# Performance work log

Measured on AMD Instinct MI355X. Metric: run time of the kernel, lower is better.

Reference implementation:

```python
import jax, jax.numpy as jnp
import numpy as np

EMBED = 2048
HEADS = 16
GROUPS = 4
HEAD_DIM = EMBED // HEADS  # 128
REPEATS = HEADS // GROUPS  # 4


def setup_inputs() -> dict:
    key = jax.random.key(0)
    ks = jax.random.split(key, 9)
    s = 1.0 / np.sqrt(EMBED)
    kv_dim = GROUPS * HEAD_DIM
    return {
        "x": jax.random.normal(ks[0], (2, 2048, EMBED), dtype=jnp.float32),
        "Wq": jax.random.normal(ks[1], (EMBED, EMBED), dtype=jnp.float32) * s,
        "bq": jnp.zeros((EMBED,), dtype=jnp.float32),
        "Wk": jax.random.normal(ks[2], (EMBED, kv_dim), dtype=jnp.float32) * s,
        "bk": jnp.zeros((kv_dim,), dtype=jnp.float32),
        "Wv": jax.random.normal(ks[3], (EMBED, kv_dim), dtype=jnp.float32) * s,
        "bv": jnp.zeros((kv_dim,), dtype=jnp.float32),
        "Wo": jax.random.normal(ks[4], (EMBED, EMBED), dtype=jnp.float32) * s,
        "bo": jnp.zeros((EMBED,), dtype=jnp.float32),
    }


def reference(x, Wq, bq, Wk, bk, Wv, bv, Wo, bo):
    b, t, e = x.shape
    q = x @ Wq + bq                                   # [b,t,e]
    k = x @ Wk + bk                                   # [b,t,g*d]
    v = x @ Wv + bv
    # [b, g, r, t, d] for q; [b, g, t, d] for k,v (repeat_interleave == group-major)
    q = q.reshape(b, t, GROUPS, REPEATS, HEAD_DIM).transpose(0, 2, 3, 1, 4)
    k = k.reshape(b, t, GROUPS, HEAD_DIM).transpose(0, 2, 1, 3)
    v = v.reshape(b, t, GROUPS, HEAD_DIM).transpose(0, 2, 1, 3)
    scale = 1.0 / np.sqrt(HEAD_DIM)
    scores = jnp.einsum('bgrqd,bgkd->bgrqk', q, k) * scale
    causal = jnp.tril(jnp.ones((t, t), dtype=bool))
    scores = jnp.where(causal, scores, -jnp.inf)
    w = jax.nn.softmax(scores, axis=-1)
    out = jnp.einsum('bgrqk,bgkd->bgrqd', w, v)       # [b,g,r,t,d]
    out = out.transpose(0, 3, 1, 2, 4).reshape(b, t, e)
    return out @ Wo + bo
```

## Files before the change

### kernel.cpp

```cpp
#include <hip/hip_runtime.h>
#include <cstdint>

typedef __bf16 bf16;
typedef __attribute__((ext_vector_type(8))) __bf16 bf16x8;
typedef __attribute__((ext_vector_type(4))) __bf16 bf16x4;
typedef __attribute__((ext_vector_type(4))) float f32x4;

__device__ __forceinline__ void load_lds16(const void* g, void* l) {
  __builtin_amdgcn_global_load_lds(
      (const __attribute__((address_space(1))) unsigned int*)g,
      (__attribute__((address_space(3))) unsigned int*)l, 16, 0, 0);
}

__device__ __forceinline__ float fast_exp2(float x) {
  float r;
  asm volatile("v_exp_f32 %0, %1" : "=v"(r) : "v"(x));
  return r;
}

template <bool OUT_F32>
__global__ __launch_bounds__(256) void gemm_bt(
    const bf16* __restrict__ A, const bf16* __restrict__ Bt,
    const float* __restrict__ bias, void* __restrict__ Cv,
    int M, int N, int K) {
  __shared__ __align__(16) bf16 sA[128 * 64];
  __shared__ __align__(16) bf16 sB[128 * 64];
  const int t = threadIdx.x;
  const int w = t >> 6, lane = t & 63;
  const int quad = lane >> 4, l16 = lane & 15;
  const int wm = (w >> 1) * 64, wn = (w & 1) * 64;
  const int bm = blockIdx.y * 128, bn = blockIdx.x * 128;

  f32x4 acc[4][4] = {};
  const int srow = lane >> 3;
  const int sg = lane & 7;

  for (int kt = 0; kt < (K >> 6); ++kt) {
    const int k0 = kt << 6;
#pragma unroll
    for (int c2 = 0; c2 < 4; ++c2) {
      int c = c2 * 4 + w;
      int row = c * 8 + srow;
      int gg = sg ^ (row & 7);
      load_lds16(A + (int64_t)(bm + row) * K + k0 + gg * 8, sA + c * 512);
      load_lds16(Bt + (int64_t)(bn + row) * K + k0 + gg * 8, sB + c * 512);
    }
    asm volatile("s_waitcnt vmcnt(0)" ::: "memory");
    __syncthreads();
#pragma unroll
    for (int ks = 0; ks < 2; ++ks) {
      bf16x8 af[4], bfr[4];
#pragma unroll
      for (int i = 0; i < 4; ++i) {
        int m = wm + i * 16 + l16;
        af[i] = *(const bf16x8*)(sA + m * 64 + (((ks * 4 + quad) ^ (l16 & 7)) * 8));
        int n = wn + i * 16 + l16;
        bfr[i] = *(const bf16x8*)(sB + n * 64 + (((ks * 4 + quad) ^ (l16 & 7)) * 8));
      }
#pragma unroll
      for (int i = 0; i < 4; ++i)
#pragma unroll
        for (int j = 0; j < 4; ++j)
          acc[i][j] = __builtin_amdgcn_mfma_f32_16x16x32_bf16(af[i], bfr[j],
                                                              acc[i][j], 0, 0, 0);
    }
    __syncthreads();
  }
#pragma unroll
  for (int i = 0; i < 4; ++i) {
    int gm = bm + wm + i * 16 + quad * 4;
#pragma unroll
    for (int j = 0; j < 4; ++j) {
      int gn = bn + wn + j * 16 + l16;
      float bvv = bias ? bias[gn] : 0.0f;
#pragma unroll
      for (int r = 0; r < 4; ++r) {
        float v = acc[i][j][r] + bvv;
        if (OUT_F32)
          ((float*)Cv)[(int64_t)(gm + r) * N + gn] = v;
        else
          ((bf16*)Cv)[(int64_t)(gm + r) * N + gn] = (bf16)v;
      }
    }
  }
}

__global__ __launch_bounds__(256, 2) void attn(
    const bf16* __restrict__ QKV, const bf16* __restrict__ Vt,
    bf16* __restrict__ Out) {
  constexpr float CC = 0.08838834764831845f * 1.44269504088896f;
  __shared__ __align__(16) bf16 sK[2][64 * 128];
  __shared__ __align__(16) bf16 sV[2][128 * 64];
  __shared__ __align__(16) bf16 sP[128 * 64];

  const int t = threadIdx.x;
  const int w = t >> 6, lane = t & 63;
  const int quad = lane >> 4, l16 = lane & 15;
  const int p = blockIdx.x, h = blockIdx.y, b = blockIdx.z;
  const int g = h >> 2;
  const int wr0 = w * 16;
  const int kbase = 2048 + g * 128;
  const bf16* vtb = Vt + (int64_t)((b * 4 + g) * 128) * 2048;
  const int rk = lane >> 4, rv = lane >> 3, sgv = lane & 7;
  const int qrow0A = p * 64, qrow0B = (31 - p) * 64;
  const int niters = 32 - p;

  bf16x8 qreg[2][4];
#pragma unroll
  for (int u = 0; u < 2; ++u) {
    int qr = (u == 0 ? qrow0A : qrow0B);
#pragma unroll
    for (int ks = 0; ks < 4; ++ks)
      qreg[u][ks] = *(const bf16x8*)(QKV +
          (int64_t)(b * 2048 + qr + wr0 + l16) * 3072 + h * 128 + ks * 32 +
          quad * 8);
  }

  f32x4 oacc[2][8] = {};
  float mrow[2] = {-3.0e38f, -3.0e38f};
  float lrow[2] = {0.f, 0.f};

  auto stage = [&](int n0, bf16* sKb, bf16* sVb) {
#pragma unroll
    for (int c2 = 0; c2 < 4; ++c2) {
      int c = c2 * 4 + w;
      int rowk = c * 4 + rk;
      int ggk = (l16 & 8) | ((l16 ^ rowk) & 7);
      load_lds16(QKV + (int64_t)(b * 2048 + n0 + rowk) * 3072 + kbase + ggk * 8,
                 sKb + c * 512);
      int rowv = c * 8 + rv;
      int ggv = sgv ^ (rowv & 7);
      load_lds16(vtb + (int64_t)rowv * 2048 + n0 + ggv * 8, sVb + c * 512);
    }
  };

  stage(0, sK[0], sV[0]);

  const int prowA = wr0 + l16;
  const int prowB = 64 + wr0 + l16;

  for (int it = 0; it < niters; ++it) {
    const int cur = it & 1;
    const int n0 = it * 64;
    bf16* sKc = sK[cur];
    bf16* sVc = sV[cur];
    const bool actA = (it <= p);

    asm volatile("s_waitcnt vmcnt(0)\n\ts_barrier" ::: "memory");
    if (it + 1 < niters) stage(n0 + 64, sK[cur ^ 1], sV[cur ^ 1]);

    f32x4 sacc[2][4] = {};
    if (actA) {
#pragma unroll
      for (int ks = 0; ks < 4; ++ks) {
        bf16x8 ak[4];
#pragma unroll
        for (int mj = 0; mj < 4; ++mj) {
          int kvr = mj * 16 + l16;
          int G = ks * 4 + quad;
          int slot = (G & 8) | ((G ^ kvr) & 7);
          ak[mj] = *(const bf16x8*)(sKc + kvr * 128 + slot * 8);
        }
#pragma unroll
        for (int mj = 0; mj < 4; ++mj) {
          sacc[0][mj] = __builtin_amdgcn_mfma_f32_16x16x32_bf16(
              ak[mj], qreg[0][ks], sacc[0][mj], 0, 0, 0);
          sacc[1][mj] = __builtin_amdgcn_mfma_f32_16x16x32_bf16(
              ak[mj], qreg[1][ks], sacc[1][mj], 0, 0, 0);
        }
      }
    } else {
#pragma unroll
      for (int ks = 0; ks < 4; ++ks) {
        bf16x8 ak[4];
#pragma unroll
        for (int mj = 0; mj < 4; ++mj) {
          int kvr = mj * 16 + l16;
          int G = ks * 4 + quad;
          int slot = (G & 8) | ((G ^ kvr) & 7);
          ak[mj] = *(const bf16x8*)(sKc + kvr * 128 + slot * 8);
        }
#pragma unroll
        for (int mj = 0; mj < 4; ++mj)
          sacc[1][mj] = __builtin_amdgcn_mfma_f32_16x16x32_bf16(
              ak[mj], qreg[1][ks], sacc[1][mj], 0, 0, 0);
      }
    }

    auto softmax_u = [&](int u, bool last, int qrow0u, int prow) {
      if (last) {
        int q = qrow0u + wr0 + l16;
#pragma unroll
        for (int mj = 0; mj < 4; ++mj)
#pragma unroll
          for (int r = 0; r < 4; ++r) {
            int kv = n0 + mj * 16 + quad * 4 + r;
            if (kv > q) sacc[u][mj][r] = -3.0e38f;
          }
      }
      f32x4 m01, m23;
#pragma unroll
      for (int r = 0; r < 4; ++r) {
        m01[r] = fmaxf(sacc[u][0][r], sacc[u][1][r]);
        m23[r] = fmaxf(sacc[u][2][r], sacc[u][3][r]);
      }
      float mx = fmaxf(fmaxf(fmaxf(m01[0], m01[1]), fmaxf(m01[2], m01[3])),
                       fmaxf(fmaxf(m23[0], m23[1]), fmaxf(m23[2], m23[3])));
      mx = fmaxf(mx, __shfl_xor(mx, 16));
      mx = fmaxf(mx, __shfl_xor(mx, 32));
      float mnew = fmaxf(mrow[u], mx);
      float alpha = fast_exp2((mrow[u] - mnew) * CC);
      float rs = 0.f;
#pragma unroll
      for (int mj = 0; mj < 4; ++mj) {
        bf16x4 p4;
#pragma unroll
        for (int r = 0; r < 4; ++r) {
          float pv = fast_exp2((sacc[u][mj][r] - mnew) * CC);
          rs += pv;
          p4[r] = (bf16)pv;
        }
        int g16 = mj * 2 + (quad >> 1);
        int off = prow * 64 + ((g16 ^ (prow & 7)) * 8) + (quad & 1) * 4;
        *(bf16x4*)(sP + off) = p4;
      }
      rs += __shfl_xor(rs, 16);
      rs += __shfl_xor(rs, 32);
      lrow[u] = lrow[u] * alpha + rs;
      mrow[u] = mnew;
#pragma unroll
      for (int dj = 0; dj < 8; ++dj)
#pragma unroll
        for (int r = 0; r < 4; ++r) oacc[u][dj][r] *= alpha;
    };
    if (actA) softmax_u(0, it == p, qrow0A, prowA);
    softmax_u(1, it == niters - 1, qrow0B, prowB);

    asm volatile("s_waitcnt lgkmcnt(0)" ::: "memory");

#pragma unroll
    for (int ks2 = 0; ks2 < 2; ++ks2) {
      int G = ks2 * 4 + quad;
      bf16x8 bpA, bpB;
      if (actA)
        bpA = *(const bf16x8*)(sP + prowA * 64 + ((G ^ (prowA & 7)) * 8));
      bpB = *(const bf16x8*)(sP + prowB * 64 + ((G ^ (prowB & 7)) * 8));
      bf16x8 av[8];
#pragma unroll
      for (int dj = 0; dj < 8; ++dj) {
        int d = dj * 16 + l16;
        av[dj] = *(const bf16x8*)(sVc + d * 64 + ((G ^ (d & 7)) * 8));
      }
      if (actA) {
#pragma unroll
        for (int dj = 0; dj < 8; ++dj) {
          oacc[0][dj] = __builtin_amdgcn_mfma_f32_16x16x32_bf16(
              av[dj], bpA, oacc[0][dj], 0, 0, 0);
          oacc[1][dj] = __builtin_amdgcn_mfma_f32_16x16x32_bf16(
              av[dj], bpB, oacc[1][dj], 0, 0, 0);
        }
      } else {
#pragma unroll
        for (int dj = 0; dj < 8; ++dj)
          oacc[1][dj] = __builtin_amdgcn_mfma_f32_16x16x32_bf16(
              av[dj], bpB, oacc[1][dj], 0, 0, 0);
      }
    }
  }

#pragma unroll
  for (int u = 0; u < 2; ++u) {
    int qrow0u = (u == 0 ? qrow0A : qrow0B);
    float inv = 1.0f / lrow[u];
    int64_t grow = b * 2048 + qrow0u + wr0 + l16;
#pragma unroll
    for (int dj = 0; dj < 8; ++dj) {
      bf16x4 o4;
#pragma unroll
      for (int r = 0; r < 4; ++r) o4[r] = (bf16)(oacc[u][dj][r] * inv);
      *(bf16x4*)(Out + grow * 2048 + h * 128 + dj * 16 + quad * 4) = o4;
    }
  }
}

__device__ __forceinline__ void tr_tile(const float* __restrict__ W,
                                        bf16* __restrict__ Wt, int K, int N,
                                        int bx, int by, int t, float* tile) {
  int tx = t & 63, ty = t >> 6;
#pragma unroll
  for (int q2 = 0; q2 < 16; ++q2) {
    int r = ty + q2 * 4;
    tile[r * 65 + tx] = W[(int64_t)(by * 64 + r) * N + bx * 64 + tx];
  }
  __syncthreads();
#pragma unroll
  for (int q2 = 0; q2 < 16; ++q2) {
    int n = ty + q2 * 4;
    Wt[(int64_t)(bx * 64 + n) * K + by * 64 + tx] = (bf16)tile[tx * 65 + n];
  }
}

__global__ __launch_bounds__(256) void prep(
    const float* __restrict__ x, const float* __restrict__ Wq,
    const float* __restrict__ Wk, const float* __restrict__ Wv,
    const float* __restrict__ Wo, const float* __restrict__ bq,
    const float* __restrict__ bk, const float* __restrict__ bv,
    bf16* __restrict__ xb, bf16* __restrict__ wqkvT, bf16* __restrict__ woT,
    float* __restrict__ bqkv) {
  __shared__ float tile[64 * 65];
  const int bid = blockIdx.x;
  const int t = threadIdx.x;
  if (bid < 8192) {
    int idx = bid * 256 + t;
    float4 v = ((const float4*)x)[idx];
    bf16x4 o = {(bf16)v.x, (bf16)v.y, (bf16)v.z, (bf16)v.w};
    ((bf16x4*)xb)[idx] = o;
  } else if (bid < 8192 + 1024) {
    int b2 = bid - 8192;
    tr_tile(Wq, wqkvT, 2048, 2048, b2 & 31, b2 >> 5, t, tile);
  } else if (bid < 8192 + 1024 + 256) {
    int b2 = bid - (8192 + 1024);
    tr_tile(Wk, wqkvT + 2048 * 2048, 2048, 512, b2 & 7, b2 >> 3, t, tile);
  } else if (bid < 8192 + 1024 + 512) {
    int b2 = bid - (8192 + 1024 + 256);
    tr_tile(Wv, wqkvT + 2560 * 2048, 2048, 512, b2 & 7, b2 >> 3, t, tile);
  } else if (bid < 8192 + 1024 + 512 + 1024) {
    int b2 = bid - (8192 + 1024 + 512);
    tr_tile(Wo, woT, 2048, 2048, b2 & 31, b2 >> 5, t, tile);
  } else {
    int i = (bid - (8192 + 1024 + 512 + 1024)) * 256 + t;
    if (i < 3072)
      bqkv[i] = i < 2048 ? bq[i] : (i < 2560 ? bk[i - 2048] : bv[i - 2560]);
  }
}

__global__ void transpose_v(const bf16* __restrict__ QKV, bf16* __restrict__ Vt) {
  __shared__ bf16 tile[32][34];
  int dt = blockIdx.x, tt = blockIdx.y, bg = blockIdx.z;
  int b = bg >> 2, g = bg & 3;
  int tx = threadIdx.x, ty = threadIdx.y;
#pragma unroll
  for (int q2 = 0; q2 < 4; ++q2) {
    int trow = tt * 32 + ty + q2 * 8;
    tile[ty + q2 * 8][tx] =
        QKV[(int64_t)(b * 2048 + trow) * 3072 + 2560 + g * 128 + dt * 32 + tx];
  }
  __syncthreads();
#pragma unroll
  for (int q2 = 0; q2 < 4; ++q2) {
    int d = dt * 32 + ty + q2 * 8;
    Vt[(int64_t)(bg * 128 + d) * 2048 + tt * 32 + tx] = tile[tx][ty + q2 * 8];
  }
}

extern "C" void kernel_launch(void* const* d_in, const int* in_sizes, int n_in,
                              void* d_out, int out_size, void* d_ws,
                              size_t ws_size, hipStream_t stream) {
  const float* x = (const float*)d_in[0];
  const float* Wq = (const float*)d_in[1];
  const float* bq = (const float*)d_in[2];
  const float* Wk = (const float*)d_in[3];
  const float* bk = (const float*)d_in[4];
  const float* Wv = (const float*)d_in[5];
  const float* bv = (const float*)d_in[6];
  const float* Wo = (const float*)d_in[7];
  const float* bo = (const float*)d_in[8];
  float* out = (float*)d_out;

  char* ws = (char*)d_ws;
  bf16* xb = (bf16*)(ws);
  bf16* wqkvT = (bf16*)(ws + 16777216);
  bf16* woT = (bf16*)(ws + 29360128);
  float* bqkv = (float*)(ws + 37748736);
  bf16* qkv = (bf16*)(ws + 37761024);
  bf16* vt = (bf16*)(ws + 62926848);
  bf16* attnb = (bf16*)(ws + 67121152);

  prep<<<8192 + 1024 + 512 + 1024 + 12, 256, 0, stream>>>(
      x, Wq, Wk, Wv, Wo, bq, bk, bv, xb, wqkvT, woT, bqkv);

  gemm_bt<false><<<dim3(24, 32), 256, 0, stream>>>(xb, wqkvT, bqkv, qkv, 4096,
                                                   3072, 2048);
  transpose_v<<<dim3(4, 64, 8), dim3(32, 8), 0, stream>>>(qkv, vt);
  attn<<<dim3(16, 16, 2), 256, 0, stream>>>(qkv, vt, attnb);
  gemm_bt<true><<<dim3(16, 32), 256, 0, stream>>>(attnb, woT, bo, out, 4096,
                                                  2048, 2048);
}
```

Measured before the change: 306.4 us.

## Keep P in registers, lazy rescale, prescaled Q, setprio, and GEMM block swizzle

The attention kernel stops writing P to shared memory. Each lane keeps its softmax probabilities in registers and feeds them to 16x16x16 bf16 MFMAs against V read from LDS, which drops the sP round-trip and the lgkmcnt wait. Q is prescaled by softmax scale times log2(e) when loaded, and the running max and rescale of O are skipped unless the new max exceeds the old one by a threshold. The kernel also adds s_setprio around the MFMA blocks and reverses the p ordering for batch 1. The GEMM gets an XCD-aware block index remap. The trade-offs are the smaller K=16 MFMA, rounding Q to bf16 after scaling, and the bounded growth allowed by lazy rescaling.

```diff
diff --git a/kernel.cpp b/kernel.cpp
--- a/kernel.cpp
+++ b/kernel.cpp
@@ -5,6 +5,7 @@
 typedef __attribute__((ext_vector_type(8))) __bf16 bf16x8;
 typedef __attribute__((ext_vector_type(4))) __bf16 bf16x4;
 typedef __attribute__((ext_vector_type(4))) float f32x4;
+typedef __attribute__((ext_vector_type(4))) short short4_t;
 
 __device__ __forceinline__ void load_lds16(const void* g, void* l) {
   __builtin_amdgcn_global_load_lds(
@@ -29,7 +30,11 @@
   const int w = t >> 6, lane = t & 63;
   const int quad = lane >> 4, l16 = lane & 15;
   const int wm = (w >> 1) * 64, wn = (w & 1) * 64;
-  const int bm = blockIdx.y * 128, bn = blockIdx.x * 128;
+  const int nbx = gridDim.x;
+  const int nwg = nbx * gridDim.y;
+  const int orig = blockIdx.y * nbx + blockIdx.x;
+  const int id = (orig & 7) * (nwg >> 3) + (orig >> 3);
+  const int bm = (id / nbx) * 128, bn = (id % nbx) * 128;
 
   f32x4 acc[4][4] = {};
   const int srow = lane >> 3;
@@ -91,12 +96,12 @@
   constexpr float CC = 0.08838834764831845f * 1.44269504088896f;
   __shared__ __align__(16) bf16 sK[2][64 * 128];
   __shared__ __align__(16) bf16 sV[2][128 * 64];
-  __shared__ __align__(16) bf16 sP[128 * 64];
 
   const int t = threadIdx.x;
   const int w = t >> 6, lane = t & 63;
   const int quad = lane >> 4, l16 = lane & 15;
-  const int p = blockIdx.x, h = blockIdx.y, b = blockIdx.z;
+  const int h = blockIdx.y, b = blockIdx.z;
+  const int p = (b == 0) ? (int)blockIdx.x : 15 - (int)blockIdx.x;
   const int g = h >> 2;
   const int wr0 = w * 16;
   const int kbase = 2048 + g * 128;
@@ -104,21 +109,6 @@
   const int rk = lane >> 4, rv = lane >> 3, sgv = lane & 7;
   const int qrow0A = p * 64, qrow0B = (31 - p) * 64;
   const int niters = 32 - p;
-
-  bf16x8 qreg[2][4];
-#pragma unroll
-  for (int u = 0; u < 2; ++u) {
-    int qr = (u == 0 ? qrow0A : qrow0B);
-#pragma unroll
-    for (int ks = 0; ks < 4; ++ks)
-      qreg[u][ks] = *(const bf16x8*)(QKV +
-          (int64_t)(b * 2048 + qr + wr0 + l16) * 3072 + h * 128 + ks * 32 +
-          quad * 8);
-  }
-
-  f32x4 oacc[2][8] = {};
-  float mrow[2] = {-3.0e38f, -3.0e38f};
-  float lrow[2] = {0.f, 0.f};
 
   auto stage = [&](int n0, bf16* sKb, bf16* sVb) {
 #pragma unroll
@@ -136,8 +126,24 @@
 
   stage(0, sK[0], sV[0]);
 
-  const int prowA = wr0 + l16;
-  const int prowB = 64 + wr0 + l16;
+  bf16x8 qreg[2][4];
+#pragma unroll
+  for (int u = 0; u < 2; ++u) {
+    int qr = (u == 0 ? qrow0A : qrow0B);
+#pragma unroll
+    for (int ks = 0; ks < 4; ++ks) {
+      bf16x8 v = *(const bf16x8*)(QKV +
+          (int64_t)(b * 2048 + qr + wr0 + l16) * 3072 + h * 128 + ks * 32 +
+          quad * 8);
+#pragma unroll
+      for (int e = 0; e < 8; ++e) v[e] = (bf16)((float)v[e] * CC);
+      qreg[u][ks] = v;
+    }
+  }
+
+  f32x4 oacc[2][8] = {};
+  float mrow[2] = {-3.0e38f, -3.0e38f};
+  float lrow[2] = {0.f, 0.f};
 
   for (int it = 0; it < niters; ++it) {
     const int cur = it & 1;
@@ -161,6 +167,7 @@
           int slot = (G & 8) | ((G ^ kvr) & 7);
           ak[mj] = *(const bf16x8*)(sKc + kvr * 128 + slot * 8);
         }
+        __builtin_amdgcn_s_setprio(1);
 #pragma unroll
         for (int mj = 0; mj < 4; ++mj) {
           sacc[0][mj] = __builtin_amdgcn_mfma_f32_16x16x32_bf16(
@@ -168,6 +175,7 @@
           sacc[1][mj] = __builtin_amdgcn_mfma_f32_16x16x32_bf16(
               ak[mj], qreg[1][ks], sacc[1][mj], 0, 0, 0);
         }
+        __builtin_amdgcn_s_setprio(0);
       }
     } else {
 #pragma unroll
@@ -180,22 +188,25 @@
           int slot = (G & 8) | ((G ^ kvr) & 7);
           ak[mj] = *(const bf16x8*)(sKc + kvr * 128 + slot * 8);
         }
+        __builtin_amdgcn_s_setprio(1);
 #pragma unroll
         for (int mj = 0; mj < 4; ++mj)
           sacc[1][mj] = __builtin_amdgcn_mfma_f32_16x16x32_bf16(
               ak[mj], qreg[1][ks], sacc[1][mj], 0, 0, 0);
-      }
-    }
-
-    auto softmax_u = [&](int u, bool last, int qrow0u, int prow) {
+        __builtin_amdgcn_s_setprio(0);
+      }
+    }
+
+    short4_t pb[2][4];
+    auto softmax_u = [&](int u, bool last, int qrow0u) {
       if (last) {
-        int q = qrow0u + wr0 + l16;
+        int qg = qrow0u + wr0 + l16;
 #pragma unroll
         for (int mj = 0; mj < 4; ++mj)
 #pragma unroll
           for (int r = 0; r < 4; ++r) {
             int kv = n0 + mj * 16 + quad * 4 + r;
-            if (kv > q) sacc[u][mj][r] = -3.0e38f;
+            if (kv > qg) sacc[u][mj][r] = -3.0e38f;
           }
       }
       f32x4 m01, m23;
@@ -208,63 +219,61 @@
                        fmaxf(fmaxf(m23[0], m23[1]), fmaxf(m23[2], m23[3])));
       mx = fmaxf(mx, __shfl_xor(mx, 16));
       mx = fmaxf(mx, __shfl_xor(mx, 32));
-      float mnew = fmaxf(mrow[u], mx);
-      float alpha = fast_exp2((mrow[u] - mnew) * CC);
+      if (!__all(mx <= mrow[u] + 11.0f)) {
+        float mnew = fmaxf(mrow[u], mx);
+        float alpha = fast_exp2(mrow[u] - mnew);
+        lrow[u] *= alpha;
+#pragma unroll
+        for (int dj = 0; dj < 8; ++dj)
+#pragma unroll
+          for (int r = 0; r < 4; ++r) oacc[u][dj][r] *= alpha;
+        mrow[u] = mnew;
+      }
       float rs = 0.f;
 #pragma unroll
       for (int mj = 0; mj < 4; ++mj) {
         bf16x4 p4;
 #pragma unroll
         for (int r = 0; r < 4; ++r) {
-          float pv = fast_exp2((sacc[u][mj][r] - mnew) * CC);
+          float pv = fast_exp2(sacc[u][mj][r] - mrow[u]);
           rs += pv;
           p4[r] = (bf16)pv;
         }
-        int g16 = mj * 2 + (quad >> 1);
-        int off = prow * 64 + ((g16 ^ (prow & 7)) * 8) + (quad & 1) * 4;
-        *(bf16x4*)(sP + off) = p4;
+        pb[u][mj] = __builtin_bit_cast(short4_t, p4);
       }
       rs += __shfl_xor(rs, 16);
       rs += __shfl_xor(rs, 32);
-      lrow[u] = lrow[u] * alpha + rs;
-      mrow[u] = mnew;
-#pragma unroll
-      for (int dj = 0; dj < 8; ++dj)
-#pragma unroll
-        for (int r = 0; r < 4; ++r) oacc[u][dj][r] *= alpha;
+      lrow[u] += rs;
     };
-    if (actA) softmax_u(0, it == p, qrow0A, prowA);
-    softmax_u(1, it == niters - 1, qrow0B, prowB);
-
-    asm volatile("s_waitcnt lgkmcnt(0)" ::: "memory");
-
-#pragma unroll
-    for (int ks2 = 0; ks2 < 2; ++ks2) {
-      int G = ks2 * 4 + quad;
-      bf16x8 bpA, bpB;
-      if (actA)
-        bpA = *(const bf16x8*)(sP + prowA * 64 + ((G ^ (prowA & 7)) * 8));
-      bpB = *(const bf16x8*)(sP + prowB * 64 + ((G ^ (prowB & 7)) * 8));
-      bf16x8 av[8];
+    if (actA) softmax_u(0, it == p, qrow0A);
+    softmax_u(1, it == niters - 1, qrow0B);
+
+#pragma unroll
+    for (int mj = 0; mj < 4; ++mj) {
+      const int sbase = mj * 2 + (quad >> 1);
+      const int soff = (quad & 1) * 4;
+      short4_t av[8];
 #pragma unroll
       for (int dj = 0; dj < 8; ++dj) {
         int d = dj * 16 + l16;
-        av[dj] = *(const bf16x8*)(sVc + d * 64 + ((G ^ (d & 7)) * 8));
-      }
+        av[dj] = *(const short4_t*)(sVc + d * 64 + ((sbase ^ (d & 7)) * 8) + soff);
+      }
+      __builtin_amdgcn_s_setprio(1);
       if (actA) {
 #pragma unroll
         for (int dj = 0; dj < 8; ++dj) {
-          oacc[0][dj] = __builtin_amdgcn_mfma_f32_16x16x32_bf16(
-              av[dj], bpA, oacc[0][dj], 0, 0, 0);
-          oacc[1][dj] = __builtin_amdgcn_mfma_f32_16x16x32_bf16(
-              av[dj], bpB, oacc[1][dj], 0, 0, 0);
+          oacc[0][dj] = __builtin_amdgcn_mfma_f32_16x16x16bf16_1k(
+              av[dj], pb[0][mj], oacc[0][dj], 0, 0, 0);
+          oacc[1][dj] = __builtin_amdgcn_mfma_f32_16x16x16bf16_1k(
+              av[dj], pb[1][mj], oacc[1][dj], 0, 0, 0);
         }
       } else {
 #pragma unroll
         for (int dj = 0; dj < 8; ++dj)
-          oacc[1][dj] = __builtin_amdgcn_mfma_f32_16x16x32_bf16(
-              av[dj], bpB, oacc[1][dj], 0, 0, 0);
-      }
+          oacc[1][dj] = __builtin_amdgcn_mfma_f32_16x16x16bf16_1k(
+              av[dj], pb[1][mj], oacc[1][dj], 0, 0, 0);
+      }
+      __builtin_amdgcn_s_setprio(0);
     }
   }
 
```

After: 308.2 us. About the same (+0.6%).
